# Optimization experiments

Measured on AMD Instinct MI355X. Metric: run time of the kernel, lower is better.

The kernel has to match this reference:

```python
import jax, jax.numpy as jnp
import numpy as np

B, T, D_IN = 32, 512, 150
D, L, H = 512, 8, 8
HD = D // H
FF = 4 * D
LLM = 512
TXT = 20


def _layernorm(x, g, b, eps=1e-5):
    m = jnp.mean(x, -1, keepdims=True)
    v = jnp.var(x, -1, keepdims=True)
    return (x - m) * jax.lax.rsqrt(v + eps) * g + b


def _timestep_pe(t, d):
    # sinusoidal PE of the diffusion step, interleaved sin/cos (torch PositionalEncoding)
    pos = t.astype(jnp.float32)[:, None]
    div = jnp.exp(-jnp.log(10000.0) * jnp.arange(0, d, 2, dtype=jnp.float32) / d)
    ang = pos * div
    return jnp.stack([jnp.sin(ang), jnp.cos(ang)], -1).reshape(t.shape[0], d)


def _rope_cos_sin(t, hd):
    inv = 1.0 / (10000.0 ** (jnp.arange(0, hd, 2, dtype=jnp.float32) / hd))
    ang = jnp.arange(t, dtype=jnp.float32)[:, None] * inv  # [T, hd/2]
    ang = jnp.concatenate([ang, ang], -1)  # [T, hd]
    return jnp.cos(ang), jnp.sin(ang)


def _apply_rope(x, cos, sin):
    # x: [B,H,T,hd]; rotate-half convention
    x1, x2 = jnp.split(x, 2, -1)
    rot = jnp.concatenate([-x2, x1], -1)
    return x * cos + rot * sin


def setup_inputs() -> dict:
    key = jax.random.key(0)
    ks = iter(jax.random.split(key, 64))
    nrm = lambda shape: jax.random.normal(next(ks), shape, jnp.float32) * 0.02
    return {
        "x": jax.random.normal(next(ks), (B, T, D_IN), jnp.float32),
        "timesteps": jax.random.randint(next(ks), (B,), 0, 1000),
        "enc_text": jax.random.normal(next(ks), (B, TXT, LLM), jnp.float32),
        "W_in": nrm((D_IN, D)), "b_in": jnp.zeros((D,), jnp.float32),
        "W_t1": nrm((D, D)), "b_t1": jnp.zeros((D,), jnp.float32),
        "W_t2": nrm((D, D)), "b_t2": jnp.zeros((D,), jnp.float32),
        "W_txt": nrm((LLM, D)), "b_txt": jnp.zeros((D,), jnp.float32),
        "ln1_g": jnp.ones((L, D), jnp.float32), "ln1_b": jnp.zeros((L, D), jnp.float32),
        "Wqkv": nrm((L, D, 3 * D)), "bqkv": jnp.zeros((L, 3 * D), jnp.float32),
        "Wo": nrm((L, D, D)), "bo": jnp.zeros((L, D), jnp.float32),
        "ln2_g": jnp.ones((L, D), jnp.float32), "ln2_b": jnp.zeros((L, D), jnp.float32),
        "W1": nrm((L, D, FF)), "b1": jnp.zeros((L, FF), jnp.float32),
        "W2": nrm((L, FF, D)), "b2": jnp.zeros((L, D), jnp.float32),
        "W_out": nrm((D, D_IN)), "b_out": jnp.zeros((D_IN,), jnp.float32),
    }


def reference(x, timesteps, enc_text, W_in, b_in, W_t1, b_t1, W_t2, b_t2,
              W_txt, b_txt, ln1_g, ln1_b, Wqkv, bqkv, Wo, bo,
              ln2_g, ln2_b, W1, b1, W2, b2, W_out, b_out):
    # conditioning fusion: timestep PE -> SiLU MLP, text mean-pool -> linear, summed
    t_emb = _timestep_pe(timesteps, D)
    t_emb = jax.nn.silu(t_emb @ W_t1 + b_t1) @ W_t2 + b_t2  # [B,D]
    txt_emb = jnp.mean(enc_text, axis=1) @ W_txt + b_txt      # [B,D]
    emb = t_emb + txt_emb
    # input process + broadcast conditioning over frames (RoPE carries positions)
    h = x @ W_in + b_in + emb[:, None, :]  # [B,T,D]
    cos, sin = _rope_cos_sin(T, HD)
    scale = 1.0 / jnp.sqrt(jnp.float32(HD))
    for i in range(L):  # 8 structurally identical pre-LN RoPE encoder blocks
        y = _layernorm(h, ln1_g[i], ln1_b[i])
        q, k, v = jnp.split(y @ Wqkv[i] + bqkv[i], 3, -1)
        q = q.reshape(B, T, H, HD).transpose(0, 2, 1, 3)
        k = k.reshape(B, T, H, HD).transpose(0, 2, 1, 3)
        v = v.reshape(B, T, H, HD).transpose(0, 2, 1, 3)
        q = _apply_rope(q, cos, sin)
        k = _apply_rope(k, cos, sin)
        attn = jax.nn.softmax(jnp.einsum('bhqd,bhkd->bhqk', q, k) * scale, -1)
        o = jnp.einsum('bhqk,bhkd->bhqd', attn, v).transpose(0, 2, 1, 3).reshape(B, T, D)
        h = h + o @ Wo[i] + bo[i]
        y = _layernorm(h, ln2_g[i], ln2_b[i])
        h = h + jax.nn.gelu(y @ W1[i] + b1[i], approximate=False) @ W2[i] + b2[i]
    return h @ W_out + b_out  # [B,T,input_feats]
```

## Files before the change

kernel.cpp:

```cpp
#include <hip/hip_runtime.h>
#include <hip/hip_bf16.h>
#include <math.h>

typedef unsigned short u16;
typedef __attribute__((ext_vector_type(8))) short bf16x8;
typedef __attribute__((ext_vector_type(4))) float f32x4;

__device__ __forceinline__ u16 f2b(float x) {
  union { float f; unsigned u; } c; c.f = x;
  unsigned r = c.u + 0x7FFFu + ((c.u >> 16) & 1u);
  return (u16)(r >> 16);
}
__device__ __forceinline__ float b2f(u16 u) {
  union { unsigned u; float f; } c; c.u = ((unsigned)u) << 16;
  return c.f;
}

__device__ __forceinline__ void gl_lds16(const u16* g, u16* l) {
  __builtin_amdgcn_global_load_lds(
      (const __attribute__((address_space(1))) void*)g,
      (__attribute__((address_space(3))) void*)l, 16, 0, 0);
}

__global__ void tconv(const float* __restrict__ W, u16* __restrict__ WT,
                      int K, int N, int KApad, int Npad) {
  __shared__ float tile[32][33];
  int z = blockIdx.z;
  W += (size_t)z * K * N;
  WT += (size_t)z * Npad * KApad;
  int n0 = blockIdx.x * 32, k0 = blockIdx.y * 32;
  int tx = threadIdx.x, ty = threadIdx.y;
  for (int i = 0; i < 4; ++i) {
    int k = k0 + ty + i * 8, n = n0 + tx;
    tile[ty + i * 8][tx] = (k < K && n < N) ? W[(size_t)k * N + n] : 0.f;
  }
  __syncthreads();
  for (int i = 0; i < 4; ++i) {
    int n = n0 + ty + i * 8, k = k0 + tx;
    WT[(size_t)n * KApad + k] = f2b(tile[tx][ty + i * 8]);
  }
}

__global__ void cond1(const int* __restrict__ ts, const float* __restrict__ Wt1,
                      const float* __restrict__ bt1, float* __restrict__ t1) {
  __shared__ float pe[512];
  int b = blockIdx.x, tid = threadIdx.x;
  float pos = (float)ts[b];
  int i2 = tid >> 1;
  float dv = expf(-0.0359778920780e0f * (float)i2);
  float ang = pos * dv;
  pe[tid] = (tid & 1) ? cosf(ang) : sinf(ang);
  __syncthreads();
  float acc = bt1[tid];
  for (int k = 0; k < 512; ++k) acc += pe[k] * Wt1[k * 512 + tid];
  t1[b * 512 + tid] = acc / (1.f + expf(-acc));
}

__global__ void cond2(const float* __restrict__ t1buf, const float* __restrict__ Wt2,
                      const float* __restrict__ bt2, const float* __restrict__ enc,
                      const float* __restrict__ Wtxt, const float* __restrict__ btxt,
                      float* __restrict__ emb) {
  __shared__ float a[512], m[512];
  int b = blockIdx.x, tid = threadIdx.x;
  a[tid] = t1buf[b * 512 + tid];
  float s = 0.f;
  for (int j = 0; j < 20; ++j) s += enc[((size_t)(b * 20 + j)) * 512 + tid];
  m[tid] = s * 0.05f;
  __syncthreads();
  float acc = bt2[tid] + btxt[tid];
  for (int k = 0; k < 512; ++k) acc += a[k] * Wt2[k * 512 + tid] + m[k] * Wtxt[k * 512 + tid];
  emb[b * 512 + tid] = acc;
}

__global__ void rope_tab(float2* __restrict__ rt) {
  int idx = blockIdx.x * 256 + threadIdx.x;
  int t = idx >> 5, i = idx & 31;
  float ang = (float)t * __expf(-0.28782313662f * (float)i);
  float sn, cn;
  sincosf(ang, &sn, &cn);
  rt[idx] = make_float2(cn, sn);
}

__global__ void xconv(const float* __restrict__ x, u16* __restrict__ xb) {
  int idx = blockIdx.x * 256 + threadIdx.x;
  int mrow = idx / 192, kk = idx - mrow * 192;
  float v = (kk < 150) ? x[(size_t)mrow * 150 + kk] : 0.f;
  xb[idx] = f2b(v);
}

__global__ __launch_bounds__(256) void ln_kernel(const float* __restrict__ h,
                                                 const float* __restrict__ g,
                                                 const float* __restrict__ be,
                                                 u16* __restrict__ y) {
  int w = threadIdx.x >> 6, lane = threadIdx.x & 63;
  int row = blockIdx.x * 4 + w;
  const float* hr = h + (size_t)row * 512 + lane * 8;
  float4 a = ((const float4*)hr)[0], b4 = ((const float4*)hr)[1];
  float s = a.x + a.y + a.z + a.w + b4.x + b4.y + b4.z + b4.w;
  float s2 = a.x * a.x + a.y * a.y + a.z * a.z + a.w * a.w +
             b4.x * b4.x + b4.y * b4.y + b4.z * b4.z + b4.w * b4.w;
#pragma unroll
  for (int o = 32; o; o >>= 1) {
    s += __shfl_xor(s, o, 64);
    s2 += __shfl_xor(s2, o, 64);
  }
  float mean = s * (1.f / 512.f);
  float var = s2 * (1.f / 512.f) - mean * mean;
  float rs = rsqrtf(var + 1e-5f);
  const float4* gp = (const float4*)(g + lane * 8);
  const float4* bp = (const float4*)(be + lane * 8);
  float4 g0 = gp[0], g1 = gp[1], be0 = bp[0], be1 = bp[1];
  ushort4 o0, o1;
  o0.x = f2b((a.x - mean) * rs * g0.x + be0.x);
  o0.y = f2b((a.y - mean) * rs * g0.y + be0.y);
  o0.z = f2b((a.z - mean) * rs * g0.z + be0.z);
  o0.w = f2b((a.w - mean) * rs * g0.w + be0.w);
  o1.x = f2b((b4.x - mean) * rs * g1.x + be1.x);
  o1.y = f2b((b4.y - mean) * rs * g1.y + be1.y);
  o1.z = f2b((b4.z - mean) * rs * g1.z + be1.z);
  o1.w = f2b((b4.w - mean) * rs * g1.w + be1.w);
  ushort4* yp = (ushort4*)(y + (size_t)row * 512 + lane * 8);
  yp[0] = o0;
  yp[1] = o1;
}

__global__ __launch_bounds__(256) void attn_mfma2(const u16* __restrict__ qk,
                                                  const u16* __restrict__ vt,
                                                  u16* __restrict__ o) {
  __shared__ u16 KVs[128 * 64];
  __shared__ u16 Ps[64 * 128];
  const int tid = threadIdx.x;
  int bid = blockIdx.x;
  const int rr = bid & 7, gg = bid >> 3;
  const int qt = gg & 7;
  const int hb = rr + 8 * (gg >> 3);
  const int h = hb & 7, b = hb >> 3;
  const int lane = tid & 63, w = tid >> 6;
  const int q = lane >> 4, c16 = lane & 15;

  const size_t qbase = (size_t)(b * 512 + qt * 64) * 1024 + h * 64;
  bf16x8 q_reg[2];
  {
    int row = w * 16 + c16;
#pragma unroll
    for (int ka = 0; ka < 2; ++ka)
      q_reg[ka] = *(const bf16x8*)(qk + qbase + (size_t)row * 1024 + (ka * 4 + q) * 8);
  }

  f32x4 o_acc[4];
  float l_st[4];
#pragma unroll
  for (int jd = 0; jd < 4; ++jd) o_acc[jd] = (f32x4){0.f, 0.f, 0.f, 0.f};
#pragma unroll
  for (int r = 0; r < 4; ++r) l_st[r] = 0.f;

  const size_t kbase = (size_t)b * 512 * 1024 + 512 + h * 64;
  const size_t vtbase = ((size_t)(b * 8 + h) * 64) * 512;

  for (int kt = 0; kt < 4; ++kt) {
    if (kt) __syncthreads();
    {
      int row0 = tid >> 3, cs = tid & 7;
#pragma unroll
      for (int rep = 0; rep < 4; ++rep) {
        int r2 = rep * 32 + row0;
        int g = cs ^ (r2 & 7);
        gl_lds16(qk + kbase + (size_t)(kt * 128 + r2) * 1024 + g * 8,
                 KVs + rep * 2048 + tid * 8);
      }
    }
    __syncthreads();

    f32x4 s_acc[8];
#pragma unroll
    for (int j = 0; j < 8; ++j) s_acc[j] = (f32x4){0.f, 0.f, 0.f, 0.f};
#pragma unroll
    for (int ka = 0; ka < 2; ++ka) {
      bf16x8 bf[8];
#pragma unroll
      for (int j = 0; j < 8; ++j) {
        int row = j * 16 + c16;
        bf[j] = *(const bf16x8*)(KVs + row * 64 + (((ka * 4 + q) ^ (row & 7)) * 8));
      }
#pragma unroll
      for (int j = 0; j < 8; ++j)
        s_acc[j] = __builtin_amdgcn_mfma_f32_16x16x32_bf16(q_reg[ka], bf[j], s_acc[j], 0, 0, 0);
    }
    __syncthreads();

    {
      int vr0 = tid >> 4, cc = tid & 15;
#pragma unroll
      for (int rep = 0; rep < 4; ++rep) {
        int row = rep * 16 + vr0;
        int g2 = cc ^ (row & 15);
        gl_lds16(vt + vtbase + (size_t)row * 512 + kt * 128 + g2 * 8,
                 KVs + rep * 2048 + tid * 8);
      }
    }

#pragma unroll
    for (int r = 0; r < 4; ++r) {
      float sum = 0.f;
#pragma unroll
      for (int j = 0; j < 8; ++j) {
        float p = __expf(s_acc[j][r]);
        s_acc[j][r] = p;
        sum += p;
      }
      l_st[r] += sum;
    }

#pragma unroll
    for (int j = 0; j < 8; ++j)
#pragma unroll
      for (int r = 0; r < 4; ++r) {
        int prow = w * 16 + q * 4 + r;
        int col = j * 16 + c16;
        int cp = col >> 3;
        Ps[prow * 128 + ((cp ^ (prow & 15)) * 8) + (col & 7)] = f2b(s_acc[j][r]);
      }
    __syncthreads();

#pragma unroll
    for (int s = 0; s < 4; ++s) {
      bf16x8 af, bv[4];
      {
        int row = w * 16 + c16;
        af = *(const bf16x8*)(Ps + row * 128 + (((s * 4 + q) ^ (row & 15)) * 8));
      }
#pragma unroll
      for (int jd = 0; jd < 4; ++jd) {
        int row = jd * 16 + c16;
        bv[jd] = *(const bf16x8*)(KVs + row * 128 + (((s * 4 + q) ^ (row & 15)) * 8));
      }
#pragma unroll
      for (int jd = 0; jd < 4; ++jd)
        o_acc[jd] = __builtin_amdgcn_mfma_f32_16x16x32_bf16(af, bv[jd], o_acc[jd], 0, 0, 0);
    }
  }

#pragma unroll
  for (int r = 0; r < 4; ++r) {
    float l = l_st[r];
    l += __shfl_xor(l, 1, 64);
    l += __shfl_xor(l, 2, 64);
    l += __shfl_xor(l, 4, 64);
    l += __shfl_xor(l, 8, 64);
    float inv = 1.f / l;
    int trow = qt * 64 + w * 16 + q * 4 + r;
#pragma unroll
    for (int jd = 0; jd < 4; ++jd)
      o[(size_t)(b * 512 + trow) * 512 + h * 64 + jd * 16 + c16] = f2b(o_acc[jd][r] * inv);
  }
}

template <int MODE, int BM = 128, int BN = 128>
__global__ __launch_bounds__(256) void gemm_bf16(
    const u16* __restrict__ A, const u16* __restrict__ BT,
    const float* __restrict__ bias, const float* aux, void* aux2, void* Cout,
    int KA, int ldc, int nx) {
  __shared__ u16 As[BM * 64];
  __shared__ u16 Bs[BN * 64];
  constexpr int AI = BM / 32;
  constexpr int BJ = BN / 32;
  const int tid = threadIdx.x;
  int bid = blockIdx.x;
  int rr = bid & 7, gg = bid >> 3;
  int xN = gg % nx, yM = rr + 8 * (gg / nx);
  const int tileN = xN * BN;
  const int tileM = yM * BM;
  const int lane = tid & 63, w = tid >> 6;
  const int mw = (w >> 1) * (BM / 2), nw = (w & 1) * (BN / 2);
  const int q = lane >> 4, c16 = lane & 15;

  f32x4 acc[AI][BJ];
#pragma unroll
  for (int i = 0; i < AI; ++i)
#pragma unroll
    for (int j = 0; j < BJ; ++j) acc[i][j] = (f32x4){0.f, 0.f, 0.f, 0.f};

  const int rowA0 = tid >> 3;
  const int cs = tid & 7;
  const int KT = KA >> 6;
  for (int kt = 0; kt < KT; ++kt) {
    __syncthreads();
#pragma unroll
    for (int rep = 0; rep < BM / 32; ++rep) {
      int row = rep * 32 + rowA0;
      int g = cs ^ (row & 7);
      gl_lds16(A + (size_t)(tileM + row) * KA + kt * 64 + g * 8,
               (u16*)((char*)As + rep * 4096 + tid * 16));
    }
#pragma unroll
    for (int rep = 0; rep < BN / 32; ++rep) {
      int row = rep * 32 + rowA0;
      int g = cs ^ (row & 7);
      gl_lds16(BT + (size_t)(tileN + row) * KA + kt * 64 + g * 8,
               (u16*)((char*)Bs + rep * 4096 + tid * 16));
    }
    __syncthreads();
#pragma unroll
    for (int ks = 0; ks < 2; ++ks) {
      bf16x8 af[AI], bfr[BJ];
#pragma unroll
      for (int i = 0; i < AI; ++i) {
        int m = mw + i * 16 + c16;
        int ca = (ks * 4 + q) ^ (m & 7);
        af[i] = *(const bf16x8*)((const char*)As + m * 128 + ca * 16);
      }
#pragma unroll
      for (int j = 0; j < BJ; ++j) {
        int n = nw + j * 16 + c16;
        int cb = (ks * 4 + q) ^ (n & 7);
        bfr[j] = *(const bf16x8*)((const char*)Bs + n * 128 + cb * 16);
      }
#pragma unroll
      for (int i = 0; i < AI; ++i)
#pragma unroll
        for (int j = 0; j < BJ; ++j)
          acc[i][j] = __builtin_amdgcn_mfma_f32_16x16x32_bf16(af[i], bfr[j], acc[i][j], 0, 0, 0);
    }
  }

  if constexpr (MODE == 5) {
    const float2* rt = (const float2*)aux;
    u16* qk = (u16*)Cout;
    u16* vtp = (u16*)aux2;
#pragma unroll
    for (int i = 0; i < AI; ++i) {
      int row = tileM + mw + i * 16 + q * 4;
      int bb = row >> 9, t0 = row & 511;
#pragma unroll
      for (int jp = 0; jp < 2; ++jp) {
        int colA = tileN + nw + jp * 16 + c16;
        if (colA < 1024) {
          int colB = colA + 32;
          int d31 = colA & 31;
          float scl = (colA < 512) ? 0.125f : 1.f;
          float bA = bias[colA], bB = bias[colB];
#pragma unroll
          for (int r = 0; r < 4; ++r) {
            float2 cs2 = rt[(t0 + r) * 32 + d31];
            float x1 = acc[i][jp][r] + bA;
            float x2 = acc[i][jp + 2][r] + bB;
            size_t rbase = (size_t)(row + r) * 1024;
            qk[rbase + colA] = f2b((x1 * cs2.x - x2 * cs2.y) * scl);
            qk[rbase + colB] = f2b((x2 * cs2.x + x1 * cs2.y) * scl);
          }
        } else {
#pragma unroll
          for (int jj = jp; jj < 4; jj += 2) {
            int col = tileN + nw + jj * 16 + c16;
            int hh = (col - 1024) >> 6, d = col & 63;
            float bv2 = bias[col];
            ushort4 pk;
            pk.x = f2b(acc[i][jj][0] + bv2);
            pk.y = f2b(acc[i][jj][1] + bv2);
            pk.z = f2b(acc[i][jj][2] + bv2);
            pk.w = f2b(acc[i][jj][3] + bv2);
            *(ushort4*)(vtp + ((size_t)((bb * 8 + hh) * 64 + d)) * 512 + t0) = pk;
          }
        }
      }
    }
    return;
  }

#pragma unroll
  for (int i = 0; i < AI; ++i) {
#pragma unroll
    for (int j = 0; j < BJ; ++j) {
      int col = tileN + nw + j * 16 + c16;
      float bv = (MODE == 4) ? 0.f : bias[col];
#pragma unroll
      for (int r = 0; r < 4; ++r) {
        int row = tileM + mw + i * 16 + q * 4 + r;
        float v = acc[i][j][r] + bv;
        if (MODE == 0) {
          ((float*)Cout)[(size_t)row * ldc + col] = v + aux[(row >> 9) * 512 + col];
        } else if (MODE == 2) {
          size_t idx = (size_t)row * ldc + col;
          ((float*)Cout)[idx] = aux[idx] + v;
        } else if (MODE == 3) {
          float u = v * v;
          float p = __builtin_fmaf(0.044715f, u, 1.0f);
          float t2 = v * p;
          float e = __expf(-1.59576912f * t2);
          float r2 = __builtin_amdgcn_rcpf(1.0f + e);
          ((u16*)Cout)[(size_t)row * ldc + col] = f2b(v * r2);
        } else if (MODE == 4) {
          if (col < 150) ((float*)Cout)[(size_t)row * 150 + col] = acc[i][j][r] + bias[col];
        } else if (MODE == 6) {
          size_t idx = (size_t)row * ldc + col;
          float v2 = aux[idx] + v;
          ((float*)Cout)[idx] = v2;
          ((u16*)aux2)[idx] = f2b(v2);
        }
      }
    }
  }
}

extern "C" void kernel_launch(void* const* d_in, const int* in_sizes, int n_in,
                              void* d_out, int out_size, void* d_ws, size_t ws_size,
                              hipStream_t stream) {
  const float* x = (const float*)d_in[0];
  const int* tsteps = (const int*)d_in[1];
  const float* enc = (const float*)d_in[2];
  const float* W_in = (const float*)d_in[3];
  const float* b_in = (const float*)d_in[4];
  const float* W_t1 = (const float*)d_in[5];
  const float* b_t1 = (const float*)d_in[6];
  const float* W_t2 = (const float*)d_in[7];
  const float* b_t2 = (const float*)d_in[8];
  const float* W_txt = (const float*)d_in[9];
  const float* b_txt = (const float*)d_in[10];
  const float* ln1_g = (const float*)d_in[11];
  const float* ln1_b = (const float*)d_in[12];
  const float* Wqkv = (const float*)d_in[13];
  const float* bqkv = (const float*)d_in[14];
  const float* Wo = (const float*)d_in[15];
  const float* bo = (const float*)d_in[16];
  const float* ln2_g = (const float*)d_in[17];
  const float* ln2_b = (const float*)d_in[18];
  const float* W1 = (const float*)d_in[19];
  const float* b1 = (const float*)d_in[20];
  const float* W2 = (const float*)d_in[21];
  const float* b2 = (const float*)d_in[22];
  const float* W_out = (const float*)d_in[23];
  const float* b_out = (const float*)d_in[24];

  char* ws = (char*)d_ws;
  u16* WT_in = (u16*)(ws + 0);
  u16* WT_qkv = (u16*)(ws + 196608);
  u16* WT_o = (u16*)(ws + 12779520);
  u16* WT_1 = (u16*)(ws + 16973824);
  u16* WT_2 = (u16*)(ws + 33751040);
  u16* WT_out = (u16*)(ws + 50528256);
  u16* xb = (u16*)(ws + 50790400);
  float* hf = (float*)(ws + 57081856);
  u16* yb = (u16*)(ws + 90636288);
  u16* qkvb = (u16*)(ws + 107413504);
  float2* rtab = (float2*)(ws + 107413504 + 33554432);
  u16* ob = (u16*)(ws + 157745152);
  u16* ffb = (u16*)(ws + 174522368);
  u16* hb = (u16*)(ws + 241631232);
  u16* vtb = hb;
  float* embf = (float*)(ws + 258408448);
  float* t1c = (float*)(ws + 258473984);

  dim3 tb(32, 8);
  tconv<<<dim3(16, 6, 1), tb, 0, stream>>>(W_in, WT_in, 150, 512, 192, 512);
  tconv<<<dim3(48, 16, 8), tb, 0, stream>>>(Wqkv, WT_qkv, 512, 1536, 512, 1536);
  tconv<<<dim3(16, 16, 8), tb, 0, stream>>>(Wo, WT_o, 512, 512, 512, 512);
  tconv<<<dim3(64, 16, 8), tb, 0, stream>>>(W1, WT_1, 512, 2048, 512, 2048);
  tconv<<<dim3(16, 64, 8), tb, 0, stream>>>(W2, WT_2, 2048, 512, 2048, 512);
  tconv<<<dim3(8, 16, 1), tb, 0, stream>>>(W_out, WT_out, 512, 150, 512, 256);

  cond1<<<32, 512, 0, stream>>>(tsteps, W_t1, b_t1, t1c);
  cond2<<<32, 512, 0, stream>>>(t1c, W_t2, b_t2, enc, W_txt, b_txt, embf);
  rope_tab<<<64, 256, 0, stream>>>(rtab);
  xconv<<<12288, 256, 0, stream>>>(x, xb);

  gemm_bf16<0, 64, 128><<<4 * 256, 256, 0, stream>>>(xb, WT_in, b_in, embf, nullptr, hf, 192, 512, 4);

  for (int l = 0; l < 8; ++l) {
    ln_kernel<<<4096, 256, 0, stream>>>(hf, ln1_g + l * 512, ln1_b + l * 512, yb);
    gemm_bf16<5, 128, 128><<<12 * 128, 256, 0, stream>>>(yb, WT_qkv + (size_t)l * 1536 * 512,
                                                         bqkv + l * 1536, (const float*)rtab,
                                                         vtb, qkvb, 512, 1024, 12);
    attn_mfma2<<<2048, 256, 0, stream>>>(qkvb, vtb, ob);
    gemm_bf16<2, 64, 128><<<4 * 256, 256, 0, stream>>>(ob, WT_o + (size_t)l * 512 * 512,
                                                       bo + l * 512, hf, nullptr, hf, 512, 512, 4);
    ln_kernel<<<4096, 256, 0, stream>>>(hf, ln2_g + l * 512, ln2_b + l * 512, yb);
    gemm_bf16<3, 128, 128><<<16 * 128, 256, 0, stream>>>(yb, WT_1 + (size_t)l * 2048 * 512,
                                                         b1 + l * 2048, nullptr, nullptr, ffb,
                                                         512, 2048, 16);
    if (l < 7) {
      gemm_bf16<2, 64, 128><<<4 * 256, 256, 0, stream>>>(ffb, WT_2 + (size_t)l * 512 * 2048,
                                                         b2 + l * 512, hf, nullptr, hf, 2048, 512, 4);
    } else {
      gemm_bf16<6, 64, 128><<<4 * 256, 256, 0, stream>>>(ffb, WT_2 + (size_t)l * 512 * 2048,
                                                         b2 + l * 512, hf, hb, hf, 2048, 512, 4);
    }
  }

  gemm_bf16<4, 64, 128><<<2 * 256, 256, 0, stream>>>(hb, WT_out, b_out, nullptr, nullptr, d_out, 512, 150, 2);
}
```

Measured before the change: 2.066 ms.

## Double-buffer A tile in GEMM to overlap global loads with MFMA

The GEMM main loop double-buffers the A operand in LDS. The next A tile is prefetched with global_load_lds before the current tile is computed, and partial vmcnt waits replace full __syncthreads. The B tile stays single-buffered and is loaded after a post-compute barrier. The aim is to hide global-to-LDS latency behind MFMA work, at the cost of doubled A LDS usage, which may lower occupancy. Correctness now depends on hand-written waitcnt counts.

```diff
diff --git a/kernel.cpp b/kernel.cpp
--- a/kernel.cpp
+++ b/kernel.cpp
@@ -260,10 +260,12 @@
     const u16* __restrict__ A, const u16* __restrict__ BT,
     const float* __restrict__ bias, const float* aux, void* aux2, void* Cout,
     int KA, int ldc, int nx) {
-  __shared__ u16 As[BM * 64];
+  __shared__ u16 As[2 * BM * 64];
   __shared__ u16 Bs[BN * 64];
   constexpr int AI = BM / 32;
   constexpr int BJ = BN / 32;
+  constexpr int AREP = BM / 32;
+  constexpr int ABYTES = BM * 128;
   const int tid = threadIdx.x;
   int bid = blockIdx.x;
   int rr = bid & 7, gg = bid >> 3;
@@ -283,23 +285,41 @@
   const int rowA0 = tid >> 3;
   const int cs = tid & 7;
   const int KT = KA >> 6;
-  for (int kt = 0; kt < KT; ++kt) {
-    __syncthreads();
-#pragma unroll
-    for (int rep = 0; rep < BM / 32; ++rep) {
+
+  auto stageA = [&](int ktv, int half) {
+#pragma unroll
+    for (int rep = 0; rep < AREP; ++rep) {
       int row = rep * 32 + rowA0;
       int g = cs ^ (row & 7);
-      gl_lds16(A + (size_t)(tileM + row) * KA + kt * 64 + g * 8,
-               (u16*)((char*)As + rep * 4096 + tid * 16));
-    }
+      gl_lds16(A + (size_t)(tileM + row) * KA + ktv * 64 + g * 8,
+               (u16*)((char*)As + half * ABYTES + rep * 4096 + tid * 16));
+    }
+  };
+  auto stageB = [&](int ktv) {
 #pragma unroll
     for (int rep = 0; rep < BN / 32; ++rep) {
       int row = rep * 32 + rowA0;
       int g = cs ^ (row & 7);
-      gl_lds16(BT + (size_t)(tileN + row) * KA + kt * 64 + g * 8,
+      gl_lds16(BT + (size_t)(tileN + row) * KA + ktv * 64 + g * 8,
                (u16*)((char*)Bs + rep * 4096 + tid * 16));
     }
-    __syncthreads();
+  };
+
+  stageA(0, 0);
+  stageB(0);
+  for (int kt = 0; kt < KT; ++kt) {
+    if (kt + 1 < KT) {
+      stageA(kt + 1, (kt + 1) & 1);
+      if constexpr (AREP == 2) {
+        asm volatile("s_waitcnt vmcnt(2)" ::: "memory");
+      } else {
+        asm volatile("s_waitcnt vmcnt(4)" ::: "memory");
+      }
+    } else {
+      asm volatile("s_waitcnt vmcnt(0)" ::: "memory");
+    }
+    __builtin_amdgcn_s_barrier();
+    const char* Ab = (const char*)As + (kt & 1) * ABYTES;
 #pragma unroll
     for (int ks = 0; ks < 2; ++ks) {
       bf16x8 af[AI], bfr[BJ];
@@ -307,7 +327,7 @@
       for (int i = 0; i < AI; ++i) {
         int m = mw + i * 16 + c16;
         int ca = (ks * 4 + q) ^ (m & 7);
-        af[i] = *(const bf16x8*)((const char*)As + m * 128 + ca * 16);
+        af[i] = *(const bf16x8*)(Ab + m * 128 + ca * 16);
       }
 #pragma unroll
       for (int j = 0; j < BJ; ++j) {
@@ -321,6 +341,9 @@
         for (int j = 0; j < BJ; ++j)
           acc[i][j] = __builtin_amdgcn_mfma_f32_16x16x32_bf16(af[i], bfr[j], acc[i][j], 0, 0, 0);
     }
+    asm volatile("s_waitcnt lgkmcnt(0)" ::: "memory");
+    __builtin_amdgcn_s_barrier();
+    if (kt + 1 < KT) stageB(kt + 1);
   }
 
   if constexpr (MODE == 5) {
```

Measured after the change: 1.952 ms. -5.5%, faster.
